# Kernel optimization log

Hardware: AMD Instinct MI355X
Metric: run time of the kernel (lower is better)

## Reference

```python
import math
import jax, jax.numpy as jnp
import numpy as np

N = 200_000      # nodes per node type (user, item)
E = 1_000_000    # edges per edge type
IN = 128
OUT = 128
H = 4
DK = OUT // H    # 32
# edge type t -> (src_node_type, dst_node_type); 0=user, 1=item
EDGE_META = ((0, 1), (1, 0))


def setup_inputs() -> dict:
    key = jax.random.key(0)
    ks = jax.random.split(key, 16)
    s_in = 1.0 / math.sqrt(IN)
    s_out = 1.0 / math.sqrt(OUT)
    s_dk = 1.0 / math.sqrt(DK)
    return {
        "x": jax.random.normal(ks[0], (2, N, IN), jnp.float32),
        "edge_index": jax.random.randint(ks[1], (2, 2, E), 0, N, jnp.int32),
        # per-node-type linear layers, stacked over node type axis
        "Wk": jax.random.normal(ks[2], (2, IN, OUT), jnp.float32) * s_in,
        "bk": jax.random.normal(ks[3], (2, OUT), jnp.float32) * 0.01,
        "Wq": jax.random.normal(ks[4], (2, IN, OUT), jnp.float32) * s_in,
        "bq": jax.random.normal(ks[5], (2, OUT), jnp.float32) * 0.01,
        "Wm": jax.random.normal(ks[6], (2, IN, OUT), jnp.float32) * s_in,
        "bm": jax.random.normal(ks[7], (2, OUT), jnp.float32) * 0.01,
        "Wa": jax.random.normal(ks[8], (2, OUT, OUT), jnp.float32) * s_out,
        "ba": jax.random.normal(ks[9], (2, OUT), jnp.float32) * 0.01,
        # per-edge-type relation params
        "w_att": jax.random.normal(ks[10], (2, H, DK, DK), jnp.float32) * s_dk,
        "w_msg": jax.random.normal(ks[11], (2, H, DK, DK), jnp.float32) * s_dk,
        "mu": jnp.ones((2, H), jnp.float32),
        # skip gates and layernorm params per node type
        "skip": jnp.ones((2,), jnp.float32),
        "ln_scale": jnp.ones((2, OUT), jnp.float32),
        "ln_bias": jnp.zeros((2, OUT), jnp.float32),
    }


def _proj(x, W, b):
    # [2,N,IN] @ [2,IN,OUT] per node type -> [2,N,H,DK]
    y = jnp.einsum("tni,tio->tno", x, W) + b[:, None, :]
    return y.reshape(2, N, H, DK)


def _hgt_forward(x, edge_index, Wk, bk, Wq, bq, Wm, bm, Wa, ba,
                 w_att, w_msg, mu, skip, ln_scale, ln_bias):
    scale = 1.0 / math.sqrt(DK)
    K = _proj(x, Wk, bk)
    Q = _proj(x, Wq, bq)
    M = _proj(x, Wm, bm)

    buckets = {}
    for t, (s, d) in enumerate(EDGE_META):
        src, dst = edge_index[t, 0], edge_index[t, 1]
        k_s = K[s][src]            # [E,H,DK] gather by src
        q_t = Q[d][dst]            # [E,H,DK] gather by dst
        m_s = M[s][src]
        k_tr = jnp.einsum("ehd,hdf->ehf", k_s, w_att[t])
        att = (k_tr * q_t).sum(-1) * mu[t] * scale      # [E,H]
        msg = jnp.einsum("ehd,hdf->ehf", m_s, w_msg[t])  # [E,H,DK]
        buckets[d] = (att, msg, dst)

    outs = []
    for nt in range(2):
        att, msg, dst = buckets[nt]
        # segment softmax over edges grouped by destination node
        seg_max = jax.ops.segment_max(att, dst, num_segments=N)   # [N,H]
        e = jnp.exp(att - seg_max[dst])
        den = jax.ops.segment_sum(e, dst, num_segments=N)         # [N,H]
        a = e / (den[dst] + 1e-16)
        agg = jax.ops.segment_sum(msg * a[..., None], dst, num_segments=N)
        agg = agg.reshape(N, OUT)
        new = jax.nn.gelu(agg, approximate=False) @ Wa[nt] + ba[nt]
        alpha = jax.nn.sigmoid(skip[nt])
        o = alpha * new + (1.0 - alpha) * x[nt]
        mean = o.mean(-1, keepdims=True)
        var = ((o - mean) ** 2).mean(-1, keepdims=True)
        o = (o - mean) * jax.lax.rsqrt(var + 1e-5) * ln_scale[nt] + ln_bias[nt]
        outs.append(o)
    return jnp.stack(outs)  # [2,N,OUT]


def reference(x, edge_index, Wk, bk, Wq, bq, Wm, bm, Wa, ba,
              w_att, w_msg, mu, skip, ln_scale, ln_bias):
    return _hgt_forward(x, edge_index, Wk, bk, Wq, bq, Wm, bm, Wa, ba,
                        w_att, w_msg, mu, skip, ln_scale, ln_bias)
```

## Files before the change

kernel.cpp:

```cpp
#include <hip/hip_runtime.h>

#define NN 200000
#define NEDGE 1000000
#define TOT (2*NN)
#define NBLK 391
#define MTILES 1563

typedef __attribute__((ext_vector_type(8))) short short8;
typedef __attribute__((ext_vector_type(4))) float floatx4;

__device__ inline float bf2f(unsigned int u) {
    unsigned int x = (u & 0xffffu) << 16;
    return __builtin_bit_cast(float, x);
}
__device__ inline unsigned int f2bf(float f) {
    unsigned int x = __builtin_bit_cast(unsigned int, f);
    x += 0x7fffu + ((x >> 16) & 1u);
    return (x >> 16) & 0xffffu;
}

__global__ void k_weights(const float* Wk, const float* bk, const float* Wq, const float* bq,
                          const float* Wm, const float* bm, const float* Wa, const float* ba,
                          const float* watt, const float* wmsg,
                          unsigned short* Wt, float* beff) {
    int t = blockIdx.x / 5, p = blockIdx.x % 5;
    int te = 1 - t;
    unsigned short* dstW = Wt + (size_t)(t*5+p)*16384;
    float* dstB = beff + (t*5+p)*128;
    for (int idx = threadIdx.x; idx < 16384; idx += blockDim.x) {
        int o = idx >> 7, i = idx & 127;
        float v;
        if (p == 0)      v = Wk[(t*128+i)*128 + o];
        else if (p == 1) v = Wm[(t*128+i)*128 + o];
        else if (p == 2) {
            int h = o >> 5, d = o & 31;
            float s = 0.f;
            for (int f = 0; f < 32; ++f)
                s += Wq[(t*128+i)*128 + h*32 + f] * watt[((te*4+h)*32+d)*32 + f];
            v = s;
        } else if (p == 3) {
            int ho = o >> 5, f = o & 31, hi = i >> 5, d = i & 31;
            v = (ho == hi) ? wmsg[((te*4+ho)*32+d)*32 + f] : 0.f;
        } else            v = Wa[(t*128+i)*128 + o];
        dstW[o*128 + i] = (unsigned short)f2bf(v);
    }
    for (int o = threadIdx.x; o < 128; o += blockDim.x) {
        float v;
        if (p == 0)      v = bk[t*128+o];
        else if (p == 1) v = bm[t*128+o];
        else if (p == 2) {
            int h = o >> 5, d = o & 31;
            float s = 0.f;
            for (int f = 0; f < 32; ++f)
                s += bq[t*128 + h*32 + f] * watt[((te*4+h)*32+d)*32 + f];
            v = s;
        } else if (p == 3) v = 0.f;
        else              v = ba[t*128+o];
        dstB[o] = v;
    }
}

__global__ void k_hist(const int* ei, int* deg) {
    int f = blockIdx.x*blockDim.x + threadIdx.x;
    if (f >= 2*NEDGE) return;
    int t = f / NEDGE, e = f - t*NEDGE;
    int dst = ei[(t*2+1)*NEDGE + e];
    atomicAdd(&deg[(1-t)*NN + dst], 1);
}

__global__ void k_scan1(const int* deg, int* offs, int* bsum) {
    __shared__ int sd[1024];
    int tid = threadIdx.x;
    int i = blockIdx.x*1024 + tid;
    int v = (i < TOT) ? deg[i] : 0;
    sd[tid] = v; __syncthreads();
    for (int o = 1; o < 1024; o <<= 1) {
        int tv = 0;
        if (tid >= o) tv = sd[tid - o];
        __syncthreads();
        if (tid >= o) sd[tid] += tv;
        __syncthreads();
    }
    if (i < TOT) offs[i] = sd[tid] - v;
    if (tid == 1023) bsum[blockIdx.x] = sd[tid];
}

__global__ void k_scan2(int* bsum) {
    __shared__ int sd[512];
    int tid = threadIdx.x;
    int v = (tid < NBLK) ? bsum[tid] : 0;
    sd[tid] = v; __syncthreads();
    for (int o = 1; o < 512; o <<= 1) {
        int tv = 0;
        if (tid >= o) tv = sd[tid - o];
        __syncthreads();
        if (tid >= o) sd[tid] += tv;
        __syncthreads();
    }
    if (tid < NBLK) bsum[tid] = sd[tid] - v;
}

__global__ void k_scan3(int* offs, const int* bsum, int* cursor) {
    int i = blockIdx.x*blockDim.x + threadIdx.x;
    if (i >= TOT) return;
    int v = offs[i] + bsum[i >> 10];
    offs[i] = v;
    cursor[i] = v;
}

__global__ void k_scatter(const int* ei, int* cursor, int* slot) {
    int f = blockIdx.x*blockDim.x + threadIdx.x;
    if (f >= 2*NEDGE) return;
    int t = f / NEDGE, e = f - t*NEDGE;
    int src = ei[(t*2+0)*NEDGE + e];
    int dst = ei[(t*2+1)*NEDGE + e];
    int pos = atomicAdd(&cursor[(1-t)*NN + dst], 1);
    slot[pos] = src;
}

__global__ __launch_bounds__(256) void k_proj(const float* x, const unsigned short* Wt,
        const float* beff, unsigned short* KM, float* Qo) {
    __shared__ __align__(16) unsigned short xs[128*136];
    __shared__ __align__(16) unsigned short ws[128*136];
    int t = blockIdx.y;
    int rowbase = blockIdx.x * 128;
    int tid = threadIdx.x;
    const float* xb = x + (size_t)t*NN*128;
    for (int it = 0; it < 16; ++it) {
        int q = it*256 + tid;
        int r = q >> 5, c = (q & 31)*4;
        int gr = rowbase + r;
        float4 v = make_float4(0.f,0.f,0.f,0.f);
        if (gr < NN) v = *(const float4*)(xb + (size_t)gr*128 + c);
        *(uint2*)(xs + r*136 + c) = make_uint2(f2bf(v.x) | (f2bf(v.y)<<16),
                                               f2bf(v.z) | (f2bf(v.w)<<16));
    }
    int wave = tid >> 6, lane = tid & 63;
    int lrow = lane & 15, quad = lane >> 4;
    unsigned short* KMb = KM + (size_t)t*NN*256;
    float* Qb = Qo + (size_t)t*NN*128;
    for (int p = 0; p < 3; ++p) {
        const unsigned short* wsrc = Wt + (size_t)(t*5+p)*16384;
        for (int it = 0; it < 8; ++it) {
            int e = (it*256+tid)*8; int r = e>>7, c = e&127;
            *(uint4*)(ws + r*136 + c) = *(const uint4*)(wsrc + r*128 + c);
        }
        __syncthreads();
        floatx4 acc[2][8];
        for (int i=0;i<2;++i) for (int j=0;j<8;++j) acc[i][j] = (floatx4){0.f,0.f,0.f,0.f};
        for (int ks = 0; ks < 4; ++ks) {
            int koff = ks*32 + quad*8;
            short8 a[2], b[8];
            for (int i=0;i<2;++i) a[i] = *(const short8*)(xs + ((wave*2+i)*16 + lrow)*136 + koff);
            for (int j=0;j<8;++j) b[j] = *(const short8*)(ws + (j*16 + lrow)*136 + koff);
            for (int i=0;i<2;++i)
                for (int j=0;j<8;++j)
                    acc[i][j] = __builtin_amdgcn_mfma_f32_16x16x32_bf16(a[i], b[j], acc[i][j], 0, 0, 0);
        }
        const float* bb = beff + (t*5+p)*128;
        for (int j=0;j<8;++j) {
            int col = j*16 + lrow;
            float bias = bb[col];
            for (int i=0;i<2;++i)
                for (int r=0;r<4;++r) {
                    int grow = rowbase + (wave*2+i)*16 + quad*4 + r;
                    if (grow < NN) {
                        float v = acc[i][j][r] + bias;
                        if (p < 2) KMb[(size_t)grow*256 + col*2 + p] = (unsigned short)f2bf(v);
                        else       Qb[(size_t)grow*128 + col] = v;
                    }
                }
        }
        __syncthreads();
    }
}

__global__ __launch_bounds__(256) void k_gather(const unsigned short* KM, float* QA,
        const int* offs, const int* deg, const int* slot, const float* mu) {
    int nt = blockIdx.y;
    int grp = threadIdx.x >> 5, ln = threadIdx.x & 31;
    int node = blockIdx.x*8 + grp;
    int s = 1 - nt;
    int head = ln >> 3;
    float* qptr = QA + ((size_t)nt*NN + node)*128 + ln*4;
    float4 q = *(const float4*)qptr;
    float mf = mu[s*4 + head] * 0.17677669529663687f;
    float q0 = q.x*mf, q1 = q.y*mf, q2 = q.z*mf, q3 = q.w*mf;
    int g = nt*NN + node;
    int st = offs[g], en = st + deg[g];
    const unsigned short* KMb = KM + (size_t)s*NN*256;
    float m = -INFINITY, l = 0.f;
    float a0=0.f, a1=0.f, a2=0.f, a3=0.f;
    for (int e = st; e < en; ++e) {
        int src = slot[e];
        uint4 km = *(const uint4*)(KMb + (size_t)src*256 + ln*8);
        float k0 = bf2f(km.x), m0 = bf2f(km.x>>16);
        float k1 = bf2f(km.y), m1 = bf2f(km.y>>16);
        float k2 = bf2f(km.z), m2 = bf2f(km.z>>16);
        float k3 = bf2f(km.w), m3 = bf2f(km.w>>16);
        float dot = k0*q0 + k1*q1 + k2*q2 + k3*q3;
        dot += __shfl_xor(dot, 1);
        dot += __shfl_xor(dot, 2);
        dot += __shfl_xor(dot, 4);
        float nm = fmaxf(m, dot);
        float pp = __expf(dot - nm);
        float sc = __expf(m - nm);
        l = l*sc + pp;
        m = nm;
        a0 = a0*sc + pp*m0;
        a1 = a1*sc + pp*m1;
        a2 = a2*sc + pp*m2;
        a3 = a3*sc + pp*m3;
    }
    if (l > 0.f) { float inv = 1.f/l; a0*=inv; a1*=inv; a2*=inv; a3*=inv; }
    *(float4*)qptr = make_float4(a0, a1, a2, a3);
}

__global__ __launch_bounds__(256) void k_epilogue(const float* x, const unsigned short* Wt,
        const float* beff, const float* skipv, const float* lns, const float* lnb, float* out) {
    __shared__ __align__(16) unsigned short gs[128*136];
    __shared__ __align__(16) unsigned short ws[128*136];
    int t = blockIdx.y;
    int rowbase = blockIdx.x * 128;
    int tid = threadIdx.x;
    float* Ob = out + (size_t)t*NN*128;
    for (int it = 0; it < 16; ++it) {
        int q = it*256 + tid;
        int r = q >> 5, c = (q & 31)*4;
        int gr = rowbase + r;
        float4 v = make_float4(0.f,0.f,0.f,0.f);
        if (gr < NN) v = *(const float4*)(Ob + (size_t)gr*128 + c);
        *(uint2*)(gs + r*136 + c) = make_uint2(f2bf(v.x) | (f2bf(v.y)<<16),
                                               f2bf(v.z) | (f2bf(v.w)<<16));
    }
    const unsigned short* w1 = Wt + (size_t)(t*5+3)*16384;
    for (int it = 0; it < 8; ++it) {
        int e = (it*256+tid)*8; int r = e>>7, c = e&127;
        *(uint4*)(ws + r*136 + c) = *(const uint4*)(w1 + r*128 + c);
    }
    __syncthreads();
    int wave = tid >> 6, lane = tid & 63;
    int lrow = lane & 15, quad = lane >> 4;
    floatx4 acc[2][8];
    for (int i=0;i<2;++i) for (int j=0;j<8;++j) acc[i][j] = (floatx4){0.f,0.f,0.f,0.f};
    for (int ks = 0; ks < 4; ++ks) {
        int koff = ks*32 + quad*8;
        short8 a[2], b[8];
        for (int i=0;i<2;++i) a[i] = *(const short8*)(gs + ((wave*2+i)*16 + lrow)*136 + koff);
        for (int j=0;j<8;++j) b[j] = *(const short8*)(ws + (j*16 + lrow)*136 + koff);
        for (int i=0;i<2;++i)
            for (int j=0;j<8;++j)
                acc[i][j] = __builtin_amdgcn_mfma_f32_16x16x32_bf16(a[i], b[j], acc[i][j], 0, 0, 0);
    }
    __syncthreads();
    for (int j=0;j<8;++j) {
        int col = j*16 + lrow;
        for (int i=0;i<2;++i)
            for (int r=0;r<4;++r) {
                int rl = (wave*2+i)*16 + quad*4 + r;
                float v = acc[i][j][r];
                v = 0.5f*v*(1.f + erff(v*0.70710678118654752f));
                gs[rl*136 + col] = (unsigned short)f2bf(v);
            }
    }
    const unsigned short* w2 = Wt + (size_t)(t*5+4)*16384;
    for (int it = 0; it < 8; ++it) {
        int e = (it*256+tid)*8; int r = e>>7, c = e&127;
        *(uint4*)(ws + r*136 + c) = *(const uint4*)(w2 + r*128 + c);
    }
    __syncthreads();
    for (int i=0;i<2;++i) for (int j=0;j<8;++j) acc[i][j] = (floatx4){0.f,0.f,0.f,0.f};
    for (int ks = 0; ks < 4; ++ks) {
        int koff = ks*32 + quad*8;
        short8 a[2], b[8];
        for (int i=0;i<2;++i) a[i] = *(const short8*)(gs + ((wave*2+i)*16 + lrow)*136 + koff);
        for (int j=0;j<8;++j) b[j] = *(const short8*)(ws + (j*16 + lrow)*136 + koff);
        for (int i=0;i<2;++i)
            for (int j=0;j<8;++j)
                acc[i][j] = __builtin_amdgcn_mfma_f32_16x16x32_bf16(a[i], b[j], acc[i][j], 0, 0, 0);
    }
    const float* bb = beff + (t*5+4)*128;
    float alpha = 1.f/(1.f + __expf(-skipv[t]));
    float beta = 1.f - alpha;
    const float* xb = x + (size_t)t*NN*128;
    for (int i=0;i<2;++i)
        for (int r=0;r<4;++r) {
            int row = rowbase + (wave*2+i)*16 + quad*4 + r;
            bool ok = row < NN;
            float o[8]; float sum = 0.f, ss = 0.f;
            for (int j=0;j<8;++j) {
                int col = j*16 + lrow;
                float xv = ok ? xb[(size_t)row*128 + col] : 0.f;
                float v = alpha*(acc[i][j][r] + bb[col]) + beta*xv;
                o[j] = v; sum += v; ss += v*v;
            }
            sum += __shfl_xor(sum, 1); sum += __shfl_xor(sum, 2);
            sum += __shfl_xor(sum, 4); sum += __shfl_xor(sum, 8);
            ss  += __shfl_xor(ss, 1);  ss  += __shfl_xor(ss, 2);
            ss  += __shfl_xor(ss, 4);  ss  += __shfl_xor(ss, 8);
            float mean = sum * (1.f/128.f);
            float var = fmaxf(ss * (1.f/128.f) - mean*mean, 0.f);
            float rstd = rsqrtf(var + 1e-5f);
            if (ok) {
                for (int j=0;j<8;++j) {
                    int col = j*16 + lrow;
                    Ob[(size_t)row*128 + col] = (o[j]-mean)*rstd*lns[t*128+col] + lnb[t*128+col];
                }
            }
        }
}

extern "C" void kernel_launch(void* const* d_in, const int* in_sizes, int n_in,
                              void* d_out, int out_size, void* d_ws, size_t ws_size,
                              hipStream_t stream) {
    const float* x    = (const float*)d_in[0];
    const int*   ei   = (const int*)d_in[1];
    const float* Wk   = (const float*)d_in[2];
    const float* bk   = (const float*)d_in[3];
    const float* Wq   = (const float*)d_in[4];
    const float* bq   = (const float*)d_in[5];
    const float* Wm   = (const float*)d_in[6];
    const float* bm   = (const float*)d_in[7];
    const float* Wa   = (const float*)d_in[8];
    const float* ba   = (const float*)d_in[9];
    const float* watt = (const float*)d_in[10];
    const float* wmsg = (const float*)d_in[11];
    const float* mu   = (const float*)d_in[12];
    const float* skp  = (const float*)d_in[13];
    const float* lns  = (const float*)d_in[14];
    const float* lnb  = (const float*)d_in[15];
    float* out = (float*)d_out;

    char* w = (char*)d_ws;
    unsigned short* Wt = (unsigned short*)(w + 0);
    float* beff        = (float*)(w + 327680);
    int* deg           = (int*)(w + 332800);
    int* offs          = (int*)(w + 1932800);
    int* cursor        = (int*)(w + 3532800);
    int* bsum          = (int*)(w + 5132800);
    int* slot          = (int*)(w + 5136896);
    unsigned short* KM = (unsigned short*)(w + 13136896);

    hipMemsetAsync(deg, 0, (size_t)TOT*4, stream);
    k_weights<<<10, 256, 0, stream>>>(Wk,bk,Wq,bq,Wm,bm,Wa,ba,watt,wmsg,Wt,beff);
    k_hist<<<(2*NEDGE+255)/256, 256, 0, stream>>>(ei, deg);
    k_scan1<<<NBLK, 1024, 0, stream>>>(deg, offs, bsum);
    k_scan2<<<1, 512, 0, stream>>>(bsum);
    k_scan3<<<(TOT+255)/256, 256, 0, stream>>>(offs, bsum, cursor);
    k_scatter<<<(2*NEDGE+255)/256, 256, 0, stream>>>(ei, cursor, slot);
    k_proj<<<dim3(MTILES,2), 256, 0, stream>>>(x, Wt, beff, KM, out);
    k_gather<<<dim3(NN/8,2), 256, 0, stream>>>(KM, out, offs, deg, slot, mu);
    k_epilogue<<<dim3(MTILES,2), 256, 0, stream>>>(x, Wt, beff, skp, lns, lnb, out);
}
```

Baseline: 1.626 ms.

## Shrink projection/epilogue tiles to 64 rows, keep A in registers, prefetch weights

Row tiles in the projection and epilogue GEMM kernels shrink from 128 to 64, which doubles the grid and cuts LDS use so more blocks fit per CU. Activation rows now load straight into MFMA A-fragments in registers instead of going through shared memory. The next weight matrix is prefetched into registers while the current one is used. K and M outputs are packed into single 32-bit stores. The cost is more weight reloads per row, since each block still loads full 128x128 weight tiles, plus higher register pressure.

```diff
diff --git a/kernel.cpp b/kernel.cpp
--- a/kernel.cpp
+++ b/kernel.cpp
@@ -4,7 +4,7 @@
 #define NEDGE 1000000
 #define TOT (2*NN)
 #define NBLK 391
-#define MTILES 1563
+#define PTILES 3125
 
 typedef __attribute__((ext_vector_type(8))) short short8;
 typedef __attribute__((ext_vector_type(4))) float floatx4;
@@ -17,6 +17,12 @@
     unsigned int x = __builtin_bit_cast(unsigned int, f);
     x += 0x7fffu + ((x >> 16) & 1u);
     return (x >> 16) & 0xffffu;
+}
+__device__ inline short8 cvt8(float4 v0, float4 v1) {
+    short8 r;
+    r[0]=(short)f2bf(v0.x); r[1]=(short)f2bf(v0.y); r[2]=(short)f2bf(v0.z); r[3]=(short)f2bf(v0.w);
+    r[4]=(short)f2bf(v1.x); r[5]=(short)f2bf(v1.y); r[6]=(short)f2bf(v1.z); r[7]=(short)f2bf(v1.w);
+    return r;
 }
 
 __global__ void k_weights(const float* Wk, const float* bk, const float* Wq, const float* bq,
@@ -118,60 +124,117 @@
     slot[pos] = src;
 }
 
-__global__ __launch_bounds__(256) void k_proj(const float* x, const unsigned short* Wt,
+#define STAGE_LOAD(reg, p) \
+    { const unsigned short* wsrc_ = Wt + (size_t)(t*5+(p))*16384; \
+      _Pragma("unroll") \
+      for (int it_ = 0; it_ < 8; ++it_) \
+          reg[it_] = *(const uint4*)(wsrc_ + (it_*256+tid)*8); }
+
+#define STAGE_WRITE(reg) \
+    { _Pragma("unroll") \
+      for (int it_ = 0; it_ < 8; ++it_) { int e_ = (it_*256+tid)*8; \
+          *(uint4*)(ws + (e_>>7)*136 + (e_&127)) = reg[it_]; } }
+
+__global__ __launch_bounds__(256, 3) void k_proj(const float* x, const unsigned short* Wt,
         const float* beff, unsigned short* KM, float* Qo) {
-    __shared__ __align__(16) unsigned short xs[128*136];
     __shared__ __align__(16) unsigned short ws[128*136];
     int t = blockIdx.y;
-    int rowbase = blockIdx.x * 128;
     int tid = threadIdx.x;
-    const float* xb = x + (size_t)t*NN*128;
-    for (int it = 0; it < 16; ++it) {
-        int q = it*256 + tid;
-        int r = q >> 5, c = (q & 31)*4;
-        int gr = rowbase + r;
-        float4 v = make_float4(0.f,0.f,0.f,0.f);
-        if (gr < NN) v = *(const float4*)(xb + (size_t)gr*128 + c);
-        *(uint2*)(xs + r*136 + c) = make_uint2(f2bf(v.x) | (f2bf(v.y)<<16),
-                                               f2bf(v.z) | (f2bf(v.w)<<16));
-    }
     int wave = tid >> 6, lane = tid & 63;
     int lrow = lane & 15, quad = lane >> 4;
+    int rowbase = blockIdx.x * 64;
+    int row = rowbase + wave*16 + lrow;
+    const float* xr = x + (size_t)t*NN*128 + (size_t)row*128 + quad*8;
+
+    float4 xv[8];
+#pragma unroll
+    for (int ks = 0; ks < 4; ++ks) {
+        xv[2*ks]   = *(const float4*)(xr + ks*32);
+        xv[2*ks+1] = *(const float4*)(xr + ks*32 + 4);
+    }
+    uint4 wreg[8];
+    STAGE_LOAD(wreg, 0);
+    short8 a[4];
+#pragma unroll
+    for (int ks = 0; ks < 4; ++ks) a[ks] = cvt8(xv[2*ks], xv[2*ks+1]);
+    STAGE_WRITE(wreg);
+    __syncthreads();
+
+    uint4 wreg2[8];
+    STAGE_LOAD(wreg2, 1);
+    floatx4 acc[8];
+#pragma unroll
+    for (int j = 0; j < 8; ++j) acc[j] = (floatx4){0.f,0.f,0.f,0.f};
+#pragma unroll
+    for (int ks = 0; ks < 4; ++ks) {
+        int koff = ks*32 + quad*8;
+#pragma unroll
+        for (int j = 0; j < 8; ++j) {
+            short8 b = *(const short8*)(ws + (j*16 + lrow)*136 + koff);
+            acc[j] = __builtin_amdgcn_mfma_f32_16x16x32_bf16(a[ks], b, acc[j], 0, 0, 0);
+        }
+    }
+    const float* bkb = beff + (t*5+0)*128;
+    unsigned int kb[8][2];
+#pragma unroll
+    for (int j = 0; j < 8; ++j) {
+        float bias = bkb[j*16 + lrow];
+        kb[j][0] = f2bf(acc[j][0]+bias) | (f2bf(acc[j][1]+bias) << 16);
+        kb[j][1] = f2bf(acc[j][2]+bias) | (f2bf(acc[j][3]+bias) << 16);
+    }
+    __syncthreads();
+    STAGE_WRITE(wreg2);
+    __syncthreads();
+
+    STAGE_LOAD(wreg, 2);
+#pragma unroll
+    for (int j = 0; j < 8; ++j) acc[j] = (floatx4){0.f,0.f,0.f,0.f};
+#pragma unroll
+    for (int ks = 0; ks < 4; ++ks) {
+        int koff = ks*32 + quad*8;
+#pragma unroll
+        for (int j = 0; j < 8; ++j) {
+            short8 b = *(const short8*)(ws + (j*16 + lrow)*136 + koff);
+            acc[j] = __builtin_amdgcn_mfma_f32_16x16x32_bf16(a[ks], b, acc[j], 0, 0, 0);
+        }
+    }
+    const float* bmb = beff + (t*5+1)*128;
     unsigned short* KMb = KM + (size_t)t*NN*256;
+    int orow = rowbase + wave*16 + quad*4;
+#pragma unroll
+    for (int j = 0; j < 8; ++j) {
+        int col = j*16 + lrow;
+        float bias = bmb[col];
+        unsigned int k01 = kb[j][0], k23 = kb[j][1];
+        *(unsigned int*)(KMb + (size_t)(orow+0)*256 + col*2) = (k01 & 0xffffu) | (f2bf(acc[j][0]+bias) << 16);
+        *(unsigned int*)(KMb + (size_t)(orow+1)*256 + col*2) = (k01 >> 16)     | (f2bf(acc[j][1]+bias) << 16);
+        *(unsigned int*)(KMb + (size_t)(orow+2)*256 + col*2) = (k23 & 0xffffu) | (f2bf(acc[j][2]+bias) << 16);
+        *(unsigned int*)(KMb + (size_t)(orow+3)*256 + col*2) = (k23 >> 16)     | (f2bf(acc[j][3]+bias) << 16);
+    }
+    __syncthreads();
+    STAGE_WRITE(wreg);
+    __syncthreads();
+
+#pragma unroll
+    for (int j = 0; j < 8; ++j) acc[j] = (floatx4){0.f,0.f,0.f,0.f};
+#pragma unroll
+    for (int ks = 0; ks < 4; ++ks) {
+        int koff = ks*32 + quad*8;
+#pragma unroll
+        for (int j = 0; j < 8; ++j) {
+            short8 b = *(const short8*)(ws + (j*16 + lrow)*136 + koff);
+            acc[j] = __builtin_amdgcn_mfma_f32_16x16x32_bf16(a[ks], b, acc[j], 0, 0, 0);
+        }
+    }
+    const float* bqb = beff + (t*5+2)*128;
     float* Qb = Qo + (size_t)t*NN*128;
-    for (int p = 0; p < 3; ++p) {
-        const unsigned short* wsrc = Wt + (size_t)(t*5+p)*16384;
-        for (int it = 0; it < 8; ++it) {
-            int e = (it*256+tid)*8; int r = e>>7, c = e&127;
-            *(uint4*)(ws + r*136 + c) = *(const uint4*)(wsrc + r*128 + c);
-        }
-        __syncthreads();
-        floatx4 acc[2][8];
-        for (int i=0;i<2;++i) for (int j=0;j<8;++j) acc[i][j] = (floatx4){0.f,0.f,0.f,0.f};
-        for (int ks = 0; ks < 4; ++ks) {
-            int koff = ks*32 + quad*8;
-            short8 a[2], b[8];
-            for (int i=0;i<2;++i) a[i] = *(const short8*)(xs + ((wave*2+i)*16 + lrow)*136 + koff);
-            for (int j=0;j<8;++j) b[j] = *(const short8*)(ws + (j*16 + lrow)*136 + koff);
-            for (int i=0;i<2;++i)
-                for (int j=0;j<8;++j)
-                    acc[i][j] = __builtin_amdgcn_mfma_f32_16x16x32_bf16(a[i], b[j], acc[i][j], 0, 0, 0);
-        }
-        const float* bb = beff + (t*5+p)*128;
-        for (int j=0;j<8;++j) {
-            int col = j*16 + lrow;
-            float bias = bb[col];
-            for (int i=0;i<2;++i)
-                for (int r=0;r<4;++r) {
-                    int grow = rowbase + (wave*2+i)*16 + quad*4 + r;
-                    if (grow < NN) {
-                        float v = acc[i][j][r] + bias;
-                        if (p < 2) KMb[(size_t)grow*256 + col*2 + p] = (unsigned short)f2bf(v);
-                        else       Qb[(size_t)grow*128 + col] = v;
-                    }
-                }
-        }
-        __syncthreads();
+#pragma unroll
+    for (int j = 0; j < 8; ++j) {
+        int col = j*16 + lrow;
+        float bias = bqb[col];
+#pragma unroll
+        for (int r = 0; r < 4; ++r)
+            Qb[(size_t)(orow+r)*128 + col] = acc[j][r] + bias;
     }
 }
 
@@ -216,98 +279,106 @@
     *(float4*)qptr = make_float4(a0, a1, a2, a3);
 }
 
-__global__ __launch_bounds__(256) void k_epilogue(const float* x, const unsigned short* Wt,
+__global__ __launch_bounds__(256, 3) void k_epilogue(const float* x, const unsigned short* Wt,
         const float* beff, const float* skipv, const float* lns, const float* lnb, float* out) {
-    __shared__ __align__(16) unsigned short gs[128*136];
     __shared__ __align__(16) unsigned short ws[128*136];
+    __shared__ __align__(16) unsigned short gs[64*136];
     int t = blockIdx.y;
-    int rowbase = blockIdx.x * 128;
     int tid = threadIdx.x;
-    float* Ob = out + (size_t)t*NN*128;
-    for (int it = 0; it < 16; ++it) {
-        int q = it*256 + tid;
-        int r = q >> 5, c = (q & 31)*4;
-        int gr = rowbase + r;
-        float4 v = make_float4(0.f,0.f,0.f,0.f);
-        if (gr < NN) v = *(const float4*)(Ob + (size_t)gr*128 + c);
-        *(uint2*)(gs + r*136 + c) = make_uint2(f2bf(v.x) | (f2bf(v.y)<<16),
-                                               f2bf(v.z) | (f2bf(v.w)<<16));
-    }
-    const unsigned short* w1 = Wt + (size_t)(t*5+3)*16384;
-    for (int it = 0; it < 8; ++it) {
-        int e = (it*256+tid)*8; int r = e>>7, c = e&127;
-        *(uint4*)(ws + r*136 + c) = *(const uint4*)(w1 + r*128 + c);
-    }
-    __syncthreads();
     int wave = tid >> 6, lane = tid & 63;
     int lrow = lane & 15, quad = lane >> 4;
-    floatx4 acc[2][8];
-    for (int i=0;i<2;++i) for (int j=0;j<8;++j) acc[i][j] = (floatx4){0.f,0.f,0.f,0.f};
+    int rowbase = blockIdx.x * 64;
+    int row = rowbase + wave*16 + lrow;
+    float* Ob = out + (size_t)t*NN*128;
+
+    const float* ar = Ob + (size_t)row*128 + quad*8;
+    float4 xv[8];
+#pragma unroll
+    for (int ks = 0; ks < 4; ++ks) {
+        xv[2*ks]   = *(const float4*)(ar + ks*32);
+        xv[2*ks+1] = *(const float4*)(ar + ks*32 + 4);
+    }
+    uint4 wreg[8];
+    STAGE_LOAD(wreg, 3);
+    short8 a[4];
+#pragma unroll
+    for (int ks = 0; ks < 4; ++ks) a[ks] = cvt8(xv[2*ks], xv[2*ks+1]);
+    STAGE_WRITE(wreg);
+    __syncthreads();
+
+    uint4 wreg2[8];
+    STAGE_LOAD(wreg2, 4);
+    floatx4 acc[8];
+#pragma unroll
+    for (int j = 0; j < 8; ++j) acc[j] = (floatx4){0.f,0.f,0.f,0.f};
+#pragma unroll
     for (int ks = 0; ks < 4; ++ks) {
         int koff = ks*32 + quad*8;
-        short8 a[2], b[8];
-        for (int i=0;i<2;++i) a[i] = *(const short8*)(gs + ((wave*2+i)*16 + lrow)*136 + koff);
-        for (int j=0;j<8;++j) b[j] = *(const short8*)(ws + (j*16 + lrow)*136 + koff);
-        for (int i=0;i<2;++i)
-            for (int j=0;j<8;++j)
-                acc[i][j] = __builtin_amdgcn_mfma_f32_16x16x32_bf16(a[i], b[j], acc[i][j], 0, 0, 0);
-    }
-    __syncthreads();
-    for (int j=0;j<8;++j) {
+#pragma unroll
+        for (int j = 0; j < 8; ++j) {
+            short8 b = *(const short8*)(ws + (j*16 + lrow)*136 + koff);
+            acc[j] = __builtin_amdgcn_mfma_f32_16x16x32_bf16(a[ks], b, acc[j], 0, 0, 0);
+        }
+    }
+#pragma unroll
+    for (int j = 0; j < 8; ++j) {
         int col = j*16 + lrow;
-        for (int i=0;i<2;++i)
-            for (int r=0;r<4;++r) {
-                int rl = (wave*2+i)*16 + quad*4 + r;
-                float v = acc[i][j][r];
-                v = 0.5f*v*(1.f + erff(v*0.70710678118654752f));
-                gs[rl*136 + col] = (unsigned short)f2bf(v);
-            }
-    }
-    const unsigned short* w2 = Wt + (size_t)(t*5+4)*16384;
-    for (int it = 0; it < 8; ++it) {
-        int e = (it*256+tid)*8; int r = e>>7, c = e&127;
-        *(uint4*)(ws + r*136 + c) = *(const uint4*)(w2 + r*128 + c);
-    }
-    __syncthreads();
-    for (int i=0;i<2;++i) for (int j=0;j<8;++j) acc[i][j] = (floatx4){0.f,0.f,0.f,0.f};
+#pragma unroll
+        for (int r = 0; r < 4; ++r) {
+            int rl = wave*16 + quad*4 + r;
+            float v = acc[j][r];
+            v = 0.5f*v*(1.f + erff(v*0.70710678118654752f));
+            gs[rl*136 + col] = (unsigned short)f2bf(v);
+        }
+    }
+    __syncthreads();
+    STAGE_WRITE(wreg2);
+    __syncthreads();
+
+    short8 a2[4];
+#pragma unroll
+    for (int ks = 0; ks < 4; ++ks)
+        a2[ks] = *(const short8*)(gs + (wave*16 + lrow)*136 + ks*32 + quad*8);
+#pragma unroll
+    for (int j = 0; j < 8; ++j) acc[j] = (floatx4){0.f,0.f,0.f,0.f};
+#pragma unroll
     for (int ks = 0; ks < 4; ++ks) {
         int koff = ks*32 + quad*8;
-        short8 a[2], b[8];
-        for (int i=0;i<2;++i) a[i] = *(const short8*)(gs + ((wave*2+i)*16 + lrow)*136 + koff);
-        for (int j=0;j<8;++j) b[j] = *(const short8*)(ws + (j*16 + lrow)*136 + koff);
-        for (int i=0;i<2;++i)
-            for (int j=0;j<8;++j)
-                acc[i][j] = __builtin_amdgcn_mfma_f32_16x16x32_bf16(a[i], b[j], acc[i][j], 0, 0, 0);
-    }
+#pragma unroll
+        for (int j = 0; j < 8; ++j) {
+            short8 b = *(const short8*)(ws + (j*16 + lrow)*136 + koff);
+            acc[j] = __builtin_amdgcn_mfma_f32_16x16x32_bf16(a2[ks], b, acc[j], 0, 0, 0);
+        }
+    }
+
     const float* bb = beff + (t*5+4)*128;
     float alpha = 1.f/(1.f + __expf(-skipv[t]));
     float beta = 1.f - alpha;
     const float* xb = x + (size_t)t*NN*128;
-    for (int i=0;i<2;++i)
-        for (int r=0;r<4;++r) {
-            int row = rowbase + (wave*2+i)*16 + quad*4 + r;
-            bool ok = row < NN;
-            float o[8]; float sum = 0.f, ss = 0.f;
-            for (int j=0;j<8;++j) {
-                int col = j*16 + lrow;
-                float xv = ok ? xb[(size_t)row*128 + col] : 0.f;
-                float v = alpha*(acc[i][j][r] + bb[col]) + beta*xv;
-                o[j] = v; sum += v; ss += v*v;
-            }
-            sum += __shfl_xor(sum, 1); sum += __shfl_xor(sum, 2);
-            sum += __shfl_xor(sum, 4); sum += __shfl_xor(sum, 8);
-            ss  += __shfl_xor(ss, 1);  ss  += __shfl_xor(ss, 2);
-            ss  += __shfl_xor(ss, 4);  ss  += __shfl_xor(ss, 8);
-            float mean = sum * (1.f/128.f);
-            float var = fmaxf(ss * (1.f/128.f) - mean*mean, 0.f);
-            float rstd = rsqrtf(var + 1e-5f);
-            if (ok) {
-                for (int j=0;j<8;++j) {
-                    int col = j*16 + lrow;
-                    Ob[(size_t)row*128 + col] = (o[j]-mean)*rstd*lns[t*128+col] + lnb[t*128+col];
-                }
-            }
-        }
+#pragma unroll
+    for (int r = 0; r < 4; ++r) {
+        int orow = rowbase + wave*16 + quad*4 + r;
+        float o[8]; float sum = 0.f, ss = 0.f;
+#pragma unroll
+        for (int j = 0; j < 8; ++j) {
+            int col = j*16 + lrow;
+            float xvv = xb[(size_t)orow*128 + col];
+            float v = alpha*(acc[j][r] + bb[col]) + beta*xvv;
+            o[j] = v; sum += v; ss += v*v;
+        }
+        sum += __shfl_xor(sum, 1); sum += __shfl_xor(sum, 2);
+        sum += __shfl_xor(sum, 4); sum += __shfl_xor(sum, 8);
+        ss  += __shfl_xor(ss, 1);  ss  += __shfl_xor(ss, 2);
+        ss  += __shfl_xor(ss, 4);  ss  += __shfl_xor(ss, 8);
+        float mean = sum * (1.f/128.f);
+        float var = fmaxf(ss * (1.f/128.f) - mean*mean, 0.f);
+        float rstd = rsqrtf(var + 1e-5f);
+#pragma unroll
+        for (int j = 0; j < 8; ++j) {
+            int col = j*16 + lrow;
+            Ob[(size_t)orow*128 + col] = (o[j]-mean)*rstd*lns[t*128+col] + lnb[t*128+col];
+        }
+    }
 }
 
 extern "C" void kernel_launch(void* const* d_in, const int* in_sizes, int n_in,
@@ -348,7 +419,7 @@
     k_scan2<<<1, 512, 0, stream>>>(bsum);
     k_scan3<<<(TOT+255)/256, 256, 0, stream>>>(offs, bsum, cursor);
     k_scatter<<<(2*NEDGE+255)/256, 256, 0, stream>>>(ei, cursor, slot);
-    k_proj<<<dim3(MTILES,2), 256, 0, stream>>>(x, Wt, beff, KM, out);
+    k_proj<<<dim3(PTILES,2), 256, 0, stream>>>(x, Wt, beff, KM, out);
     k_gather<<<dim3(NN/8,2), 256, 0, stream>>>(KM, out, offs, deg, slot, mu);
-    k_epilogue<<<dim3(MTILES,2), 256, 0, stream>>>(x, Wt, beff, skp, lns, lnb, out);
-}
+    k_epilogue<<<dim3(PTILES,2), 256, 0, stream>>>(x, Wt, beff, skp, lns, lnb, out);
+}
```

Measured after the change: 1.430 ms. 12.1% less time.
